# Kernel tuning notes

Measured on AMD Instinct MI355X. Metric: run time of the kernel, lower is better.

The kernel has to match this reference:

```python
import jax, jax.numpy as jnp
import numpy as np

N0, K3, K2 = 262144, 27, 8
N1, N2 = N0 // 8, N0 // 64
CIN, C0, C1, C2 = 3, 24, 48, 96
EPS = 1e-5


def _conv_bn_relu(x, neigh, W, gamma, beta):
    # Octree sparse conv: gather neighbor features and contract with kernel.
    # x: [N, Cin], neigh: [M, K] int indices into N, W: [K, Cin, Cout]
    y = jnp.einsum('mkc,kcd->md', x[neigh], W)
    # BatchNorm1d (training-mode batch statistics) + ReLU
    mu = jnp.mean(y, axis=0)
    var = jnp.var(y, axis=0)
    y = (y - mu) * jax.lax.rsqrt(var + EPS) * gamma + beta
    return jax.nn.relu(y)


def setup_inputs() -> dict:
    key = jax.random.key(0)
    k = jax.random.split(key, 16)

    def w(kk, shape, fan):
        return jax.random.normal(kk, shape, jnp.float32) / np.float32(np.sqrt(fan))

    return {
        'data':   jax.random.normal(k[0], (N0, CIN), jnp.float32),
        'neigh0': jax.random.randint(k[1], (N0, K3), 0, N0, jnp.int32),
        'child0': jax.random.randint(k[2], (N1, K2), 0, N0, jnp.int32),
        'neigh1': jax.random.randint(k[3], (N1, K3), 0, N1, jnp.int32),
        'child1': jax.random.randint(k[4], (N2, K2), 0, N1, jnp.int32),
        'neigh2': jax.random.randint(k[5], (N2, K3), 0, N2, jnp.int32),
        'w0':  w(k[6],  (K3, CIN, C0), K3 * CIN),
        'g0':  jnp.ones((C0,), jnp.float32),  'b0':  jnp.zeros((C0,), jnp.float32),
        'wd0': w(k[7],  (K2, C0, C1),  K2 * C0),
        'gd0': jnp.ones((C1,), jnp.float32),  'bd0': jnp.zeros((C1,), jnp.float32),
        'w1':  w(k[8],  (K3, C1, C1),  K3 * C1),
        'g1':  jnp.ones((C1,), jnp.float32),  'b1':  jnp.zeros((C1,), jnp.float32),
        'wd1': w(k[9],  (K2, C1, C2),  K2 * C1),
        'gd1': jnp.ones((C2,), jnp.float32),  'bd1': jnp.zeros((C2,), jnp.float32),
        'wp':  w(k[10], (K3, C2, C2),  K3 * C2),
        'gp':  jnp.ones((C2,), jnp.float32),  'bp':  jnp.zeros((C2,), jnp.float32),
    }


def reference(data, neigh0, child0, neigh1, child1, neigh2,
              w0, g0, b0, wd0, gd0, bd0, w1, g1, b1, wd1, gd1, bd1, wp, gp, bp):
    # stage 0 at depth d: conv3 then stride-2 downsample
    x = _conv_bn_relu(data, neigh0, w0, g0, b0)      # [N0, 24]
    x = _conv_bn_relu(x, child0, wd0, gd0, bd0)      # [N1, 48]
    # stage 1 at depth d-1
    x = _conv_bn_relu(x, neigh1, w1, g1, b1)         # [N1, 48]
    x = _conv_bn_relu(x, child1, wd1, gd1, bd1)      # [N2, 96]
    # proj at depth d-2
    x = _conv_bn_relu(x, neigh2, wp, gp, bp)         # [N2, 96]
    return x
```

## Files before the change

### kernel.cpp

```cpp
#include <hip/hip_runtime.h>

#define N0 262144
#define N1 32768
#define N2 4096
#define EPSBN 1e-5f

typedef unsigned short ush_t;
typedef __bf16 bf16x8 __attribute__((ext_vector_type(8)));
typedef float  f32x4  __attribute__((ext_vector_type(4)));

union ufcast { unsigned int u; float f; };
__device__ __forceinline__ float bflo(unsigned int p) { ufcast x; x.u = p << 16;          return x.f; }
__device__ __forceinline__ float bfhi(unsigned int p) { ufcast x; x.u = p & 0xffff0000u; return x.f; }
__device__ __forceinline__ ush_t f2bf(float f) {
    ufcast x; x.f = f;
    unsigned int u = x.u + 0x7fffu + ((x.u >> 16) & 1u);
    return (ush_t)(u >> 16);
}
__device__ __forceinline__ bf16x8 as_bf8(uint4 u) {
    union { uint4 u; bf16x8 b; } x; x.u = u; return x.b;
}

template<int C, int NB>
__device__ __forceinline__ void compute_ss(const float* __restrict__ bins,
                                           const float* __restrict__ g, const float* __restrict__ b,
                                           float M, float* ssl)
{
    const int tid = threadIdx.x;
    if (tid < 2 * C) {
        float s = 0.f;
#pragma unroll
        for (int k = 0; k < NB; ++k) s += bins[k * 2 * C + tid];
        ssl[tid] = s;
    }
    __syncthreads();
    if (tid < C) {
        const float mu  = ssl[tid] / M;
        const float var = fmaxf(ssl[C + tid] / M - mu * mu, 0.f);
        const float sc  = g[tid] / sqrtf(var + EPSBN);
        const float sh  = b[tid] - mu * sc;
        ssl[tid] = sc; ssl[C + tid] = sh;
    }
    __syncthreads();
}

template<int K, int CIN, int CINP_W, int COUT, int COUTP, int NCH>
__device__ __forceinline__ void prep_stage(const float* __restrict__ W, ush_t* __restrict__ Wb, int e) {
    const int k  = e & 31;
    const int n  = (e >> 5) % COUTP;
    const int ch = e / (32 * COUTP);
    const int kp = ch * 32 + k;
    const int t  = kp / CINP_W;
    const int c  = kp % CINP_W;
    float v = 0.f;
    if (t < K && c < CIN && n < COUT) v = W[((size_t)t * CIN + c) * COUT + n];
    Wb[e] = f2bf(v);
}

#define BINS_TOTAL 9984

__global__ __launch_bounds__(256) void prep_all(
    const float* w0, const float* wd0, const float* w1, const float* wd1, const float* wp,
    const float* data,
    ush_t* wbA, ush_t* wbB, ush_t* wbC, ush_t* wbD, ush_t* wbE, ush_t* xa, float* binsz)
{
    const int e = blockIdx.x * 256 + threadIdx.x;
    switch (blockIdx.y) {
        case 0: if (e <   4096) prep_stage<27,  3,  4, 24, 32,  4>(w0,  wbA, e); break;
        case 1: if (e <  12288) prep_stage< 8, 24, 32, 48, 48,  8>(wd0, wbB, e); break;
        case 2: if (e <  64512) prep_stage<27, 48, 48, 48, 48, 42>(w1,  wbC, e); break;
        case 3: if (e <  49152) prep_stage< 8, 48, 64, 96, 96, 16>(wd1, wbD, e); break;
        case 4: if (e < 248832) prep_stage<27, 96, 96, 96, 96, 81>(wp,  wbE, e); break;
        case 5: if (e < N0) {
            const float* dp = data + (size_t)3 * e;
            unsigned int h0 = f2bf(dp[0]), h1 = f2bf(dp[1]), h2 = f2bf(dp[2]);
            uint2 v; v.x = h0 | (h1 << 16); v.y = h2;
            ((uint2*)xa)[e] = v;
        } break;
        case 6: if (e < BINS_TOTAL) binsz[e] = 0.f; break;
    }
}

__global__ __launch_bounds__(256, 4) void mconvA_s(
    const ush_t* __restrict__ xa,
    const int*   __restrict__ neigh,
    const ush_t* __restrict__ Wb,
    ush_t*       __restrict__ y,
    float*       __restrict__ bins)
{
    __shared__ int   nl[3456];
    __shared__ float lsq[48];
    __shared__ ush_t ytile[128 * 24];
    const int tid = threadIdx.x;
    const int block0 = blockIdx.x * 128;

    {
        const uint4* src = (const uint4*)(neigh + (size_t)block0 * 27);
        uint4* dst = (uint4*)nl;
        for (int i = tid; i < 864; i += 256) dst[i] = src[i];
    }
    if (tid < 48) lsq[tid] = 0.f;
    __syncthreads();

    const int lane = tid & 63, wave = tid >> 6;
    const int quad = lane >> 4, l15 = lane & 15;

    uint4 au[2][4];
#pragma unroll
    for (int g = 0; g < 2; ++g) {
        const int lr = g * 64 + wave * 16 + l15;
#pragma unroll
        for (int ch = 0; ch < 4; ++ch) {
            const int tA = ch * 8 + quad * 2;
            uint4 a = make_uint4(0, 0, 0, 0);
            if (ch < 3) {
                const uint2 lo = ((const uint2*)xa)[nl[lr * 27 + tA]];
                const uint2 hi = ((const uint2*)xa)[nl[lr * 27 + tA + 1]];
                a = make_uint4(lo.x, lo.y, hi.x, hi.y);
            } else {
                if (quad == 0) {
                    const uint2 lo = ((const uint2*)xa)[nl[lr * 27 + 24]];
                    const uint2 hi = ((const uint2*)xa)[nl[lr * 27 + 25]];
                    a = make_uint4(lo.x, lo.y, hi.x, hi.y);
                } else if (quad == 1) {
                    const uint2 lo = ((const uint2*)xa)[nl[lr * 27 + 26]];
                    a = make_uint4(lo.x, lo.y, 0, 0);
                }
            }
            au[g][ch] = a;
        }
    }
    __builtin_amdgcn_sched_barrier(0);

    f32x4 acc[2][2] = {};
#pragma unroll
    for (int g = 0; g < 2; ++g)
#pragma unroll
    for (int ch = 0; ch < 4; ++ch) {
        const bf16x8 af = as_bf8(au[g][ch]);
#pragma unroll
        for (int ct = 0; ct < 2; ++ct) {
            const int n = ct * 16 + l15;
            const uint4 bu = *(const uint4*)(Wb + ((size_t)ch * 32 + n) * 32 + quad * 8);
            acc[g][ct] = __builtin_amdgcn_mfma_f32_16x16x32_bf16(af, as_bf8(bu), acc[g][ct], 0, 0, 0);
        }
    }

#pragma unroll
    for (int g = 0; g < 2; ++g)
#pragma unroll
    for (int ct = 0; ct < 2; ++ct) {
        const int col = ct * 16 + l15;
        if (col < 24) {
            float s = 0.f, q = 0.f;
#pragma unroll
            for (int r = 0; r < 4; ++r) {
                const float v = acc[g][ct][r];
                ytile[(g * 64 + wave * 16 + quad * 4 + r) * 24 + col] = f2bf(v);
                s += v; q += v * v;
            }
            atomicAdd(&lsq[col], s);
            atomicAdd(&lsq[24 + col], q);
        }
    }
    __syncthreads();

    {
        const uint4* t4 = (const uint4*)ytile;
        uint4* dst = (uint4*)(y + (size_t)block0 * 24);
        for (int i = tid; i < 384; i += 256) dst[i] = t4[i];
    }
    if (tid < 48) atomicAdd(&bins[(blockIdx.x & 15) * 48 + tid], lsq[tid]);
}

__global__ __launch_bounds__(256) void mconvB_s(
    const ush_t* __restrict__ y0,
    const float* __restrict__ bins0,
    const float* __restrict__ g, const float* __restrict__ b,
    const int*   __restrict__ child,
    const ush_t* __restrict__ Wb,
    ush_t*       __restrict__ y1b,
    float*       __restrict__ bins1)
{
    __shared__ float ssl[48];
    __shared__ float lsq[96];
    __shared__ ush_t ytile[64 * 48];
    const int tid = threadIdx.x;
    if (tid < 96) lsq[tid] = 0.f;
    compute_ss<24, 16>(bins0, g, b, (float)N0, ssl);

    const int lane = tid & 63, wave = tid >> 6;
    const int quad = lane >> 4, l15 = lane & 15;
    const int rowA = blockIdx.x * 64 + wave * 16 + l15;
    const int c0 = quad * 8;

    float sc[8], sh[8];
    if (c0 < 24) {
#pragma unroll
        for (int j = 0; j < 8; ++j) { sc[j] = ssl[c0 + j]; sh[j] = ssl[24 + c0 + j]; }
    }

    const int4 c4a = *(const int4*)(child + (size_t)rowA * 8);
    const int4 c4b = *(const int4*)(child + (size_t)rowA * 8 + 4);
    const int idxs[8] = {c4a.x, c4a.y, c4a.z, c4a.w, c4b.x, c4b.y, c4b.z, c4b.w};

    f32x4 acc[3] = {};
#pragma unroll
    for (int ci = 0; ci < 8; ++ci) {
        const int idx = idxs[ci];
        uint4 au = make_uint4(0, 0, 0, 0);
        if (c0 < 24) {
            const uint4 raw = *(const uint4*)(y0 + (size_t)idx * 24 + c0);
            const unsigned int w4[4] = {raw.x, raw.y, raw.z, raw.w};
            unsigned int o4[4];
#pragma unroll
            for (int h = 0; h < 4; ++h) {
                const float a0 = fmaxf(bflo(w4[h]) * sc[2 * h]     + sh[2 * h],     0.f);
                const float a1 = fmaxf(bfhi(w4[h]) * sc[2 * h + 1] + sh[2 * h + 1], 0.f);
                o4[h] = (unsigned)f2bf(a0) | ((unsigned)f2bf(a1) << 16);
            }
            au = make_uint4(o4[0], o4[1], o4[2], o4[3]);
        }
        const bf16x8 af = as_bf8(au);
#pragma unroll
        for (int ct = 0; ct < 3; ++ct) {
            const int n = ct * 16 + l15;
            const uint4 bu = *(const uint4*)(Wb + ((size_t)ci * 48 + n) * 32 + quad * 8);
            acc[ct] = __builtin_amdgcn_mfma_f32_16x16x32_bf16(af, as_bf8(bu), acc[ct], 0, 0, 0);
        }
    }

#pragma unroll
    for (int ct = 0; ct < 3; ++ct) {
        const int col = ct * 16 + l15;
        float s = 0.f, q = 0.f;
#pragma unroll
        for (int r = 0; r < 4; ++r) {
            const float v = acc[ct][r];
            ytile[(wave * 16 + quad * 4 + r) * 48 + col] = f2bf(v);
            s += v; q += v * v;
        }
        atomicAdd(&lsq[col], s);
        atomicAdd(&lsq[48 + col], q);
    }
    __syncthreads();

    {
        const uint4* t4 = (const uint4*)ytile;
        uint4* dst = (uint4*)(y1b + (size_t)blockIdx.x * 64 * 48);
        for (int i = tid; i < 384; i += 256) dst[i] = t4[i];
    }
    if (tid < 96) atomicAdd(&bins1[(blockIdx.x & 15) * 96 + tid], lsq[tid]);
}

__global__ __launch_bounds__(256) void mconvC_s(
    const ush_t* __restrict__ y1b,
    const float* __restrict__ bins1,
    const float* __restrict__ g, const float* __restrict__ b,
    const int*   __restrict__ neigh,
    const ush_t* __restrict__ Wb,
    float*       __restrict__ y2,
    float*       __restrict__ bins2)
{
    __shared__ float ssl[96];
    __shared__ float lsq[96];
    __shared__ int   nl[1728];
    __shared__ float tile[64 * 48];
    const int tid = threadIdx.x;
    if (tid < 96) lsq[tid] = 0.f;

    {
        const uint4* src = (const uint4*)(neigh + (size_t)blockIdx.x * 1728);
        uint4* dst = (uint4*)nl;
        for (int i = tid; i < 432; i += 256) dst[i] = src[i];
    }
    compute_ss<48, 16>(bins1, g, b, (float)N1, ssl);

    const int lane = tid & 63, wave = tid >> 6;
    const int quad = lane >> 4, l15 = lane & 15;
    const int rl = wave * 16 + l15;

    int coffs[3], tofs[3];
    float sc[3][8], sh[3][8];
#pragma unroll
    for (int m3 = 0; m3 < 3; ++m3) {
        const int gg = 32 * m3 + 8 * quad;
        coffs[m3] = gg % 48;
        tofs[m3]  = gg / 48;
#pragma unroll
        for (int j = 0; j < 8; ++j) { sc[m3][j] = ssl[coffs[m3] + j]; sh[m3][j] = ssl[48 + coffs[m3] + j]; }
    }

    f32x4 acc[3] = {};
    for (int cg = 0; cg < 14; ++cg) {
#pragma unroll
        for (int m3 = 0; m3 < 3; ++m3) {
            const int ch = 3 * cg + m3;
            int t = 2 * cg + tofs[m3];
            if (t > 26) t = 26;
            const int idx = nl[rl * 27 + t];
            const uint4 raw = *(const uint4*)(y1b + (size_t)idx * 48 + coffs[m3]);
            const unsigned int w4[4] = {raw.x, raw.y, raw.z, raw.w};
            unsigned int o4[4];
#pragma unroll
            for (int h = 0; h < 4; ++h) {
                const float a0 = fmaxf(bflo(w4[h]) * sc[m3][2 * h]     + sh[m3][2 * h],     0.f);
                const float a1 = fmaxf(bfhi(w4[h]) * sc[m3][2 * h + 1] + sh[m3][2 * h + 1], 0.f);
                o4[h] = (unsigned)f2bf(a0) | ((unsigned)f2bf(a1) << 16);
            }
            const bf16x8 af = as_bf8(make_uint4(o4[0], o4[1], o4[2], o4[3]));
#pragma unroll
            for (int ct = 0; ct < 3; ++ct) {
                const int n = ct * 16 + l15;
                const uint4 bu = *(const uint4*)(Wb + ((size_t)ch * 48 + n) * 32 + quad * 8);
                acc[ct] = __builtin_amdgcn_mfma_f32_16x16x32_bf16(af, as_bf8(bu), acc[ct], 0, 0, 0);
            }
        }
    }

#pragma unroll
    for (int ct = 0; ct < 3; ++ct) {
        const int col = ct * 16 + l15;
        float s = 0.f, q = 0.f;
#pragma unroll
        for (int r = 0; r < 4; ++r) {
            const float v = acc[ct][r];
            tile[(wave * 16 + quad * 4 + r) * 48 + col] = v;
            s += v; q += v * v;
        }
        atomicAdd(&lsq[col], s);
        atomicAdd(&lsq[48 + col], q);
    }
    __syncthreads();

    {
        const uint4* t4 = (const uint4*)tile;
        uint4* dst = (uint4*)(y2 + (size_t)blockIdx.x * 64 * 48);
        for (int i = tid; i < 768; i += 256) dst[i] = t4[i];
    }
    if (tid < 96) atomicAdd(&bins2[(blockIdx.x & 15) * 96 + tid], lsq[tid]);
}

__global__ __launch_bounds__(256) void mconvD_s(
    const float* __restrict__ y2, const float* __restrict__ bins2,
    const float* __restrict__ g, const float* __restrict__ b,
    const int*   __restrict__ child,
    const ush_t* __restrict__ Wb,
    float*       __restrict__ y3,
    float*       __restrict__ bins3)
{
    __shared__ float ssl[96];
    __shared__ float tile[16 * 96];
    const int tid = threadIdx.x;
    for (int i = tid; i < 1536; i += 256) tile[i] = 0.f;
    compute_ss<48, 16>(bins2, g, b, (float)N1, ssl);

    const int lane = tid & 63, wave = tid >> 6;
    const int quad = lane >> 4, l15 = lane & 15;
    const int rowA = blockIdx.x * 16 + l15;

    const int2 c2 = *(const int2*)(child + (size_t)rowA * 8 + wave * 2);

    f32x4 acc[6] = {};
#pragma unroll
    for (int u = 0; u < 4; ++u) {
        const int ci = wave * 4 + u;
        const int sub = ci & 1;
        const int idx = (u >> 1) ? c2.y : c2.x;
        const int c0 = sub * 32 + quad * 8;
        uint4 au = make_uint4(0, 0, 0, 0);
        if (c0 < 48) {
            const float4 v0 = *(const float4*)(y2 + (size_t)idx * 48 + c0);
            const float4 v1 = *(const float4*)(y2 + (size_t)idx * 48 + c0 + 4);
            const float vv[8] = {v0.x, v0.y, v0.z, v0.w, v1.x, v1.y, v1.z, v1.w};
            unsigned int o4[4];
#pragma unroll
            for (int h = 0; h < 4; ++h) {
                const float a0 = fmaxf(vv[2 * h]     * ssl[c0 + 2 * h]     + ssl[48 + c0 + 2 * h],     0.f);
                const float a1 = fmaxf(vv[2 * h + 1] * ssl[c0 + 2 * h + 1] + ssl[48 + c0 + 2 * h + 1], 0.f);
                o4[h] = (unsigned)f2bf(a0) | ((unsigned)f2bf(a1) << 16);
            }
            au = make_uint4(o4[0], o4[1], o4[2], o4[3]);
        }
        const bf16x8 af = as_bf8(au);
#pragma unroll
        for (int ct = 0; ct < 6; ++ct) {
            const int n = ct * 16 + l15;
            const uint4 bu = *(const uint4*)(Wb + ((size_t)ci * 96 + n) * 32 + quad * 8);
            acc[ct] = __builtin_amdgcn_mfma_f32_16x16x32_bf16(af, as_bf8(bu), acc[ct], 0, 0, 0);
        }
    }

#pragma unroll
    for (int ct = 0; ct < 6; ++ct)
#pragma unroll
        for (int r = 0; r < 4; ++r)
            atomicAdd(&tile[(quad * 4 + r) * 96 + ct * 16 + l15], acc[ct][r]);
    __syncthreads();

    const size_t row0 = (size_t)blockIdx.x * 16;
    for (int i = tid; i < 1536; i += 256) y3[row0 * 96 + i] = tile[i];
    if (tid < 96) {
        float s = 0.f, q = 0.f;
#pragma unroll
        for (int r = 0; r < 16; ++r) { const float v = tile[r * 96 + tid]; s += v; q += v * v; }
        atomicAdd(&bins3[(blockIdx.x & 15) * 192 + tid], s);
        atomicAdd(&bins3[(blockIdx.x & 15) * 192 + 96 + tid], q);
    }
}

__global__ __launch_bounds__(256) void mconvE_s(
    const float* __restrict__ y3, const float* __restrict__ bins3,
    const float* __restrict__ g, const float* __restrict__ b,
    const int*   __restrict__ neigh,
    const ush_t* __restrict__ Wb,
    float*       __restrict__ y4,
    float*       __restrict__ bins4)
{
    __shared__ float ssl[192];
    __shared__ float tile[16 * 96];
    __shared__ int   nl[432];
    const int tid = threadIdx.x;
    for (int i = tid; i < 1536; i += 256) tile[i] = 0.f;

    {
        const uint4* src = (const uint4*)(neigh + (size_t)blockIdx.x * 432);
        uint4* dst = (uint4*)nl;
        for (int i = tid; i < 108; i += 256) dst[i] = src[i];
    }
    compute_ss<96, 16>(bins3, g, b, (float)N2, ssl);

    const int lane = tid & 63, wave = tid >> 6;
    const int quad = lane >> 4, l15 = lane & 15;

    const int ci0 = (wave == 0) ? 0 : 21 + (wave - 1) * 20;
    const int cnt = (wave == 0) ? 21 : 20;

    f32x4 acc[6] = {};
    for (int u = 0; u < cnt; ++u) {
        const int ci = ci0 + u;
        const int t = ci / 3, sub = ci % 3;
        const int idx = nl[l15 * 27 + t];
        const int c0 = sub * 32 + quad * 8;
        const float4 v0 = *(const float4*)(y3 + (size_t)idx * 96 + c0);
        const float4 v1 = *(const float4*)(y3 + (size_t)idx * 96 + c0 + 4);
        const float vv[8] = {v0.x, v0.y, v0.z, v0.w, v1.x, v1.y, v1.z, v1.w};
        unsigned int o4[4];
#pragma unroll
        for (int h = 0; h < 4; ++h) {
            const float a0 = fmaxf(vv[2 * h]     * ssl[c0 + 2 * h]     + ssl[96 + c0 + 2 * h],     0.f);
            const float a1 = fmaxf(vv[2 * h + 1] * ssl[c0 + 2 * h + 1] + ssl[96 + c0 + 2 * h + 1], 0.f);
            o4[h] = (unsigned)f2bf(a0) | ((unsigned)f2bf(a1) << 16);
        }
        const bf16x8 af = as_bf8(make_uint4(o4[0], o4[1], o4[2], o4[3]));
#pragma unroll
        for (int ct = 0; ct < 6; ++ct) {
            const int n = ct * 16 + l15;
            const uint4 bu = *(const uint4*)(Wb + ((size_t)ci * 96 + n) * 32 + quad * 8);
            acc[ct] = __builtin_amdgcn_mfma_f32_16x16x32_bf16(af, as_bf8(bu), acc[ct], 0, 0, 0);
        }
    }

#pragma unroll
    for (int ct = 0; ct < 6; ++ct)
#pragma unroll
        for (int r = 0; r < 4; ++r)
            atomicAdd(&tile[(quad * 4 + r) * 96 + ct * 16 + l15], acc[ct][r]);
    __syncthreads();

    const size_t row0 = (size_t)blockIdx.x * 16;
    for (int i = tid; i < 1536; i += 256) y4[row0 * 96 + i] = tile[i];
    if (tid < 96) {
        float s = 0.f, q = 0.f;
#pragma unroll
        for (int r = 0; r < 16; ++r) { const float v = tile[r * 96 + tid]; s += v; q += v * v; }
        atomicAdd(&bins4[(blockIdx.x & 15) * 192 + tid], s);
        atomicAdd(&bins4[(blockIdx.x & 15) * 192 + 96 + tid], q);
    }
}

__global__ __launch_bounds__(256) void writeout_s(
    const float* __restrict__ y4, const float* __restrict__ bins4,
    const float* __restrict__ g, const float* __restrict__ b,
    float* __restrict__ out)
{
    __shared__ float ssl[192];
    compute_ss<96, 16>(bins4, g, b, (float)N2, ssl);

    const int i = (blockIdx.x * 256 + threadIdx.x) * 4;
    const int c = i % 96;
    float4 v = *(const float4*)(y4 + i);
    float4 o;
    o.x = fmaxf(v.x * ssl[c + 0] + ssl[96 + c + 0], 0.f);
    o.y = fmaxf(v.y * ssl[c + 1] + ssl[96 + c + 1], 0.f);
    o.z = fmaxf(v.z * ssl[c + 2] + ssl[96 + c + 2], 0.f);
    o.w = fmaxf(v.w * ssl[c + 3] + ssl[96 + c + 3], 0.f);
    *(float4*)(out + i) = o;
}

extern "C" void kernel_launch(void* const* d_in, const int* in_sizes, int n_in,
                              void* d_out, int out_size, void* d_ws, size_t ws_size,
                              hipStream_t stream)
{
    const float* data   = (const float*)d_in[0];
    const int*   neigh0 = (const int*)d_in[1];
    const int*   child0 = (const int*)d_in[2];
    const int*   neigh1 = (const int*)d_in[3];
    const int*   child1 = (const int*)d_in[4];
    const int*   neigh2 = (const int*)d_in[5];
    const float* w0  = (const float*)d_in[6];
    const float* g0  = (const float*)d_in[7];
    const float* b0  = (const float*)d_in[8];
    const float* wd0 = (const float*)d_in[9];
    const float* gd0 = (const float*)d_in[10];
    const float* bd0 = (const float*)d_in[11];
    const float* w1  = (const float*)d_in[12];
    const float* g1  = (const float*)d_in[13];
    const float* b1  = (const float*)d_in[14];
    const float* wd1 = (const float*)d_in[15];
    const float* gd1 = (const float*)d_in[16];
    const float* bd1 = (const float*)d_in[17];
    const float* wp  = (const float*)d_in[18];
    const float* gp  = (const float*)d_in[19];
    const float* bp  = (const float*)d_in[20];
    float* out = (float*)d_out;

    float* wsf = (float*)d_ws;
    float* bins0 = wsf;
    float* bins1 = wsf + 768;
    float* bins2 = wsf + 2304;
    float* bins3 = wsf + 3840;
    float* bins4 = wsf + 6912;

    float* Y2  = wsf + 10240;
    float* Y3  = Y2 + (size_t)1572864;
    float* Y4  = Y3 + (size_t)393216;
    ush_t* Y0B = (ush_t*)(Y4 + (size_t)393216);
    ush_t* Y1B = Y0B + (size_t)6291456;
    ush_t* XA  = Y1B + (size_t)1572864;
    ush_t* WB  = XA + (size_t)1048576;

    ush_t* wbA = WB;
    ush_t* wbB = WB + 4096;
    ush_t* wbC = WB + 16384;
    ush_t* wbD = WB + 80896;
    ush_t* wbE = WB + 130048;

    prep_all<<<dim3(1024, 7), 256, 0, stream>>>(w0, wd0, w1, wd1, wp, data,
                                                wbA, wbB, wbC, wbD, wbE, XA, wsf);

    mconvA_s<<<N0 / 128, 256, 0, stream>>>(XA, neigh0, wbA, Y0B, bins0);
    mconvB_s<<<N1 / 64, 256, 0, stream>>>(Y0B, bins0, g0, b0, child0, wbB, Y1B, bins1);
    mconvC_s<<<N1 / 64, 256, 0, stream>>>(Y1B, bins1, gd0, bd0, neigh1, wbC, Y2, bins2);
    mconvD_s<<<N2 / 16, 256, 0, stream>>>(Y2, bins2, g1, b1, child1, wbD, Y3, bins3);
    mconvE_s<<<N2 / 16, 256, 0, stream>>>(Y3, bins3, gd1, bd1, neigh2, wbE, Y4, bins4);
    writeout_s<<<N2 * 96 / 4 / 256, 256, 0, stream>>>(Y4, bins4, gp, bp, out);

    (void)in_sizes; (void)n_in; (void)out_size; (void)ws_size;
}
```

Measured before the change: 237.0 us.

## Merge later conv stages into cooperative kernels with grid-wide syncs

Replaces five separate launches (mconvB..E and writeout) with two cooperative kernels that use grid.sync() between stages, so batch-norm statistics are visible without a kernel boundary. The aim is to remove launch and drain gaps between the small late stages. It also removes a sched_barrier in mconvA. Cooperative launch requires the whole grid to be co-resident (512 blocks of 256 threads here). If the grid cannot be resident the launch fails, and grid syncs carry their own cost.

```diff
diff --git a/kernel.cpp b/kernel.cpp
--- a/kernel.cpp
+++ b/kernel.cpp
@@ -1,4 +1,7 @@
 #include <hip/hip_runtime.h>
+#include <hip/hip_cooperative_groups.h>
+
+namespace cg = cooperative_groups;
 
 #define N0 262144
 #define N1 32768
@@ -130,7 +133,6 @@
             au[g][ch] = a;
         }
     }
-    __builtin_amdgcn_sched_barrier(0);
 
     f32x4 acc[2][2] = {};
 #pragma unroll
@@ -173,329 +175,327 @@
     if (tid < 48) atomicAdd(&bins[(blockIdx.x & 15) * 48 + tid], lsq[tid]);
 }
 
-__global__ __launch_bounds__(256) void mconvB_s(
+__global__ __launch_bounds__(256) void coopBC(
     const ush_t* __restrict__ y0,
     const float* __restrict__ bins0,
-    const float* __restrict__ g, const float* __restrict__ b,
+    const float* __restrict__ gB, const float* __restrict__ bB,
     const int*   __restrict__ child,
-    const ush_t* __restrict__ Wb,
+    const ush_t* __restrict__ WbB,
     ush_t*       __restrict__ y1b,
-    float*       __restrict__ bins1)
-{
-    __shared__ float ssl[48];
-    __shared__ float lsq[96];
-    __shared__ ush_t ytile[64 * 48];
-    const int tid = threadIdx.x;
-    if (tid < 96) lsq[tid] = 0.f;
-    compute_ss<24, 16>(bins0, g, b, (float)N0, ssl);
-
-    const int lane = tid & 63, wave = tid >> 6;
-    const int quad = lane >> 4, l15 = lane & 15;
-    const int rowA = blockIdx.x * 64 + wave * 16 + l15;
-    const int c0 = quad * 8;
-
-    float sc[8], sh[8];
-    if (c0 < 24) {
-#pragma unroll
-        for (int j = 0; j < 8; ++j) { sc[j] = ssl[c0 + j]; sh[j] = ssl[24 + c0 + j]; }
-    }
-
-    const int4 c4a = *(const int4*)(child + (size_t)rowA * 8);
-    const int4 c4b = *(const int4*)(child + (size_t)rowA * 8 + 4);
-    const int idxs[8] = {c4a.x, c4a.y, c4a.z, c4a.w, c4b.x, c4b.y, c4b.z, c4b.w};
-
-    f32x4 acc[3] = {};
-#pragma unroll
-    for (int ci = 0; ci < 8; ++ci) {
-        const int idx = idxs[ci];
-        uint4 au = make_uint4(0, 0, 0, 0);
-        if (c0 < 24) {
-            const uint4 raw = *(const uint4*)(y0 + (size_t)idx * 24 + c0);
-            const unsigned int w4[4] = {raw.x, raw.y, raw.z, raw.w};
-            unsigned int o4[4];
-#pragma unroll
-            for (int h = 0; h < 4; ++h) {
-                const float a0 = fmaxf(bflo(w4[h]) * sc[2 * h]     + sh[2 * h],     0.f);
-                const float a1 = fmaxf(bfhi(w4[h]) * sc[2 * h + 1] + sh[2 * h + 1], 0.f);
-                o4[h] = (unsigned)f2bf(a0) | ((unsigned)f2bf(a1) << 16);
-            }
-            au = make_uint4(o4[0], o4[1], o4[2], o4[3]);
-        }
-        const bf16x8 af = as_bf8(au);
-#pragma unroll
-        for (int ct = 0; ct < 3; ++ct) {
-            const int n = ct * 16 + l15;
-            const uint4 bu = *(const uint4*)(Wb + ((size_t)ci * 48 + n) * 32 + quad * 8);
-            acc[ct] = __builtin_amdgcn_mfma_f32_16x16x32_bf16(af, as_bf8(bu), acc[ct], 0, 0, 0);
-        }
-    }
-
-#pragma unroll
-    for (int ct = 0; ct < 3; ++ct) {
-        const int col = ct * 16 + l15;
-        float s = 0.f, q = 0.f;
-#pragma unroll
-        for (int r = 0; r < 4; ++r) {
-            const float v = acc[ct][r];
-            ytile[(wave * 16 + quad * 4 + r) * 48 + col] = f2bf(v);
-            s += v; q += v * v;
-        }
-        atomicAdd(&lsq[col], s);
-        atomicAdd(&lsq[48 + col], q);
-    }
-    __syncthreads();
-
-    {
-        const uint4* t4 = (const uint4*)ytile;
-        uint4* dst = (uint4*)(y1b + (size_t)blockIdx.x * 64 * 48);
-        for (int i = tid; i < 384; i += 256) dst[i] = t4[i];
-    }
-    if (tid < 96) atomicAdd(&bins1[(blockIdx.x & 15) * 96 + tid], lsq[tid]);
-}
-
-__global__ __launch_bounds__(256) void mconvC_s(
-    const ush_t* __restrict__ y1b,
-    const float* __restrict__ bins1,
-    const float* __restrict__ g, const float* __restrict__ b,
+    float*       __restrict__ bins1,
+    const float* __restrict__ gC, const float* __restrict__ bC,
     const int*   __restrict__ neigh,
-    const ush_t* __restrict__ Wb,
+    const ush_t* __restrict__ WbC,
     float*       __restrict__ y2,
     float*       __restrict__ bins2)
 {
-    __shared__ float ssl[96];
-    __shared__ float lsq[96];
+    __shared__ float sslB[48];
+    __shared__ float lsqB[96];
+    __shared__ ush_t ytile[64 * 48];
+    __shared__ float sslC[96];
+    __shared__ float lsqC[96];
     __shared__ int   nl[1728];
     __shared__ float tile[64 * 48];
+
     const int tid = threadIdx.x;
-    if (tid < 96) lsq[tid] = 0.f;
-
-    {
-        const uint4* src = (const uint4*)(neigh + (size_t)blockIdx.x * 1728);
-        uint4* dst = (uint4*)nl;
-        for (int i = tid; i < 432; i += 256) dst[i] = src[i];
-    }
-    compute_ss<48, 16>(bins1, g, b, (float)N1, ssl);
-
     const int lane = tid & 63, wave = tid >> 6;
     const int quad = lane >> 4, l15 = lane & 15;
-    const int rl = wave * 16 + l15;
-
-    int coffs[3], tofs[3];
-    float sc[3][8], sh[3][8];
-#pragma unroll
-    for (int m3 = 0; m3 < 3; ++m3) {
-        const int gg = 32 * m3 + 8 * quad;
-        coffs[m3] = gg % 48;
-        tofs[m3]  = gg / 48;
-#pragma unroll
-        for (int j = 0; j < 8; ++j) { sc[m3][j] = ssl[coffs[m3] + j]; sh[m3][j] = ssl[48 + coffs[m3] + j]; }
-    }
-
-    f32x4 acc[3] = {};
-    for (int cg = 0; cg < 14; ++cg) {
-#pragma unroll
-        for (int m3 = 0; m3 < 3; ++m3) {
-            const int ch = 3 * cg + m3;
-            int t = 2 * cg + tofs[m3];
-            if (t > 26) t = 26;
-            const int idx = nl[rl * 27 + t];
-            const uint4 raw = *(const uint4*)(y1b + (size_t)idx * 48 + coffs[m3]);
-            const unsigned int w4[4] = {raw.x, raw.y, raw.z, raw.w};
-            unsigned int o4[4];
-#pragma unroll
-            for (int h = 0; h < 4; ++h) {
-                const float a0 = fmaxf(bflo(w4[h]) * sc[m3][2 * h]     + sh[m3][2 * h],     0.f);
-                const float a1 = fmaxf(bfhi(w4[h]) * sc[m3][2 * h + 1] + sh[m3][2 * h + 1], 0.f);
-                o4[h] = (unsigned)f2bf(a0) | ((unsigned)f2bf(a1) << 16);
-            }
-            const bf16x8 af = as_bf8(make_uint4(o4[0], o4[1], o4[2], o4[3]));
+
+    {
+        if (tid < 96) lsqB[tid] = 0.f;
+        compute_ss<24, 16>(bins0, gB, bB, (float)N0, sslB);
+
+        const int rowA = blockIdx.x * 64 + wave * 16 + l15;
+        const int c0 = quad * 8;
+
+        float sc[8], sh[8];
+        if (c0 < 24) {
+#pragma unroll
+            for (int j = 0; j < 8; ++j) { sc[j] = sslB[c0 + j]; sh[j] = sslB[24 + c0 + j]; }
+        }
+
+        const int4 c4a = *(const int4*)(child + (size_t)rowA * 8);
+        const int4 c4b = *(const int4*)(child + (size_t)rowA * 8 + 4);
+        const int idxs[8] = {c4a.x, c4a.y, c4a.z, c4a.w, c4b.x, c4b.y, c4b.z, c4b.w};
+
+        f32x4 acc[3] = {};
+#pragma unroll
+        for (int ci = 0; ci < 8; ++ci) {
+            const int idx = idxs[ci];
+            uint4 au = make_uint4(0, 0, 0, 0);
+            if (c0 < 24) {
+                const uint4 raw = *(const uint4*)(y0 + (size_t)idx * 24 + c0);
+                const unsigned int w4[4] = {raw.x, raw.y, raw.z, raw.w};
+                unsigned int o4[4];
+#pragma unroll
+                for (int h = 0; h < 4; ++h) {
+                    const float a0 = fmaxf(bflo(w4[h]) * sc[2 * h]     + sh[2 * h],     0.f);
+                    const float a1 = fmaxf(bfhi(w4[h]) * sc[2 * h + 1] + sh[2 * h + 1], 0.f);
+                    o4[h] = (unsigned)f2bf(a0) | ((unsigned)f2bf(a1) << 16);
+                }
+                au = make_uint4(o4[0], o4[1], o4[2], o4[3]);
+            }
+            const bf16x8 af = as_bf8(au);
 #pragma unroll
             for (int ct = 0; ct < 3; ++ct) {
                 const int n = ct * 16 + l15;
-                const uint4 bu = *(const uint4*)(Wb + ((size_t)ch * 48 + n) * 32 + quad * 8);
+                const uint4 bu = *(const uint4*)(WbB + ((size_t)ci * 48 + n) * 32 + quad * 8);
                 acc[ct] = __builtin_amdgcn_mfma_f32_16x16x32_bf16(af, as_bf8(bu), acc[ct], 0, 0, 0);
             }
         }
-    }
-
-#pragma unroll
-    for (int ct = 0; ct < 3; ++ct) {
-        const int col = ct * 16 + l15;
-        float s = 0.f, q = 0.f;
-#pragma unroll
-        for (int r = 0; r < 4; ++r) {
-            const float v = acc[ct][r];
-            tile[(wave * 16 + quad * 4 + r) * 48 + col] = v;
-            s += v; q += v * v;
-        }
-        atomicAdd(&lsq[col], s);
-        atomicAdd(&lsq[48 + col], q);
-    }
-    __syncthreads();
-
-    {
-        const uint4* t4 = (const uint4*)tile;
-        uint4* dst = (uint4*)(y2 + (size_t)blockIdx.x * 64 * 48);
-        for (int i = tid; i < 768; i += 256) dst[i] = t4[i];
-    }
-    if (tid < 96) atomicAdd(&bins2[(blockIdx.x & 15) * 96 + tid], lsq[tid]);
-}
-
-__global__ __launch_bounds__(256) void mconvD_s(
+
+#pragma unroll
+        for (int ct = 0; ct < 3; ++ct) {
+            const int col = ct * 16 + l15;
+            float s = 0.f, q = 0.f;
+#pragma unroll
+            for (int r = 0; r < 4; ++r) {
+                const float v = acc[ct][r];
+                ytile[(wave * 16 + quad * 4 + r) * 48 + col] = f2bf(v);
+                s += v; q += v * v;
+            }
+            atomicAdd(&lsqB[col], s);
+            atomicAdd(&lsqB[48 + col], q);
+        }
+        __syncthreads();
+
+        {
+            const uint4* t4 = (const uint4*)ytile;
+            uint4* dst = (uint4*)(y1b + (size_t)blockIdx.x * 64 * 48);
+            for (int i = tid; i < 384; i += 256) dst[i] = t4[i];
+        }
+        if (tid < 96) atomicAdd(&bins1[(blockIdx.x & 15) * 96 + tid], lsqB[tid]);
+    }
+
+    cg::this_grid().sync();
+
+    {
+        if (tid < 96) lsqC[tid] = 0.f;
+
+        {
+            const uint4* src = (const uint4*)(neigh + (size_t)blockIdx.x * 1728);
+            uint4* dst = (uint4*)nl;
+            for (int i = tid; i < 432; i += 256) dst[i] = src[i];
+        }
+        compute_ss<48, 16>(bins1, gC, bC, (float)N1, sslC);
+
+        const int rl = wave * 16 + l15;
+
+        int coffs[3], tofs[3];
+        float sc[3][8], sh[3][8];
+#pragma unroll
+        for (int m3 = 0; m3 < 3; ++m3) {
+            const int gg = 32 * m3 + 8 * quad;
+            coffs[m3] = gg % 48;
+            tofs[m3]  = gg / 48;
+#pragma unroll
+            for (int j = 0; j < 8; ++j) { sc[m3][j] = sslC[coffs[m3] + j]; sh[m3][j] = sslC[48 + coffs[m3] + j]; }
+        }
+
+        f32x4 acc[3] = {};
+        for (int cg2 = 0; cg2 < 14; ++cg2) {
+#pragma unroll
+            for (int m3 = 0; m3 < 3; ++m3) {
+                const int ch = 3 * cg2 + m3;
+                int t = 2 * cg2 + tofs[m3];
+                if (t > 26) t = 26;
+                const int idx = nl[rl * 27 + t];
+                const uint4 raw = *(const uint4*)(y1b + (size_t)idx * 48 + coffs[m3]);
+                const unsigned int w4[4] = {raw.x, raw.y, raw.z, raw.w};
+                unsigned int o4[4];
+#pragma unroll
+                for (int h = 0; h < 4; ++h) {
+                    const float a0 = fmaxf(bflo(w4[h]) * sc[m3][2 * h]     + sh[m3][2 * h],     0.f);
+                    const float a1 = fmaxf(bfhi(w4[h]) * sc[m3][2 * h + 1] + sh[m3][2 * h + 1], 0.f);
+                    o4[h] = (unsigned)f2bf(a0) | ((unsigned)f2bf(a1) << 16);
+                }
+                const bf16x8 af = as_bf8(make_uint4(o4[0], o4[1], o4[2], o4[3]));
+#pragma unroll
+                for (int ct = 0; ct < 3; ++ct) {
+                    const int n = ct * 16 + l15;
+                    const uint4 bu = *(const uint4*)(WbC + ((size_t)ch * 48 + n) * 32 + quad * 8);
+                    acc[ct] = __builtin_amdgcn_mfma_f32_16x16x32_bf16(af, as_bf8(bu), acc[ct], 0, 0, 0);
+                }
+            }
+        }
+
+#pragma unroll
+        for (int ct = 0; ct < 3; ++ct) {
+            const int col = ct * 16 + l15;
+            float s = 0.f, q = 0.f;
+#pragma unroll
+            for (int r = 0; r < 4; ++r) {
+                const float v = acc[ct][r];
+                tile[(wave * 16 + quad * 4 + r) * 48 + col] = v;
+                s += v; q += v * v;
+            }
+            atomicAdd(&lsqC[col], s);
+            atomicAdd(&lsqC[48 + col], q);
+        }
+        __syncthreads();
+
+        {
+            const uint4* t4 = (const uint4*)tile;
+            uint4* dst = (uint4*)(y2 + (size_t)blockIdx.x * 64 * 48);
+            for (int i = tid; i < 768; i += 256) dst[i] = t4[i];
+        }
+        if (tid < 96) atomicAdd(&bins2[(blockIdx.x & 15) * 96 + tid], lsqC[tid]);
+    }
+}
+
+__global__ __launch_bounds__(256) void coopDEW(
     const float* __restrict__ y2, const float* __restrict__ bins2,
-    const float* __restrict__ g, const float* __restrict__ b,
+    const float* __restrict__ gD, const float* __restrict__ bD,
     const int*   __restrict__ child,
-    const ush_t* __restrict__ Wb,
+    const ush_t* __restrict__ WbD,
     float*       __restrict__ y3,
-    float*       __restrict__ bins3)
-{
-    __shared__ float ssl[96];
-    __shared__ float tile[16 * 96];
-    const int tid = threadIdx.x;
-    for (int i = tid; i < 1536; i += 256) tile[i] = 0.f;
-    compute_ss<48, 16>(bins2, g, b, (float)N1, ssl);
-
-    const int lane = tid & 63, wave = tid >> 6;
-    const int quad = lane >> 4, l15 = lane & 15;
-    const int rowA = blockIdx.x * 16 + l15;
-
-    const int2 c2 = *(const int2*)(child + (size_t)rowA * 8 + wave * 2);
-
-    f32x4 acc[6] = {};
-#pragma unroll
-    for (int u = 0; u < 4; ++u) {
-        const int ci = wave * 4 + u;
-        const int sub = ci & 1;
-        const int idx = (u >> 1) ? c2.y : c2.x;
-        const int c0 = sub * 32 + quad * 8;
-        uint4 au = make_uint4(0, 0, 0, 0);
-        if (c0 < 48) {
-            const float4 v0 = *(const float4*)(y2 + (size_t)idx * 48 + c0);
-            const float4 v1 = *(const float4*)(y2 + (size_t)idx * 48 + c0 + 4);
-            const float vv[8] = {v0.x, v0.y, v0.z, v0.w, v1.x, v1.y, v1.z, v1.w};
-            unsigned int o4[4];
-#pragma unroll
-            for (int h = 0; h < 4; ++h) {
-                const float a0 = fmaxf(vv[2 * h]     * ssl[c0 + 2 * h]     + ssl[48 + c0 + 2 * h],     0.f);
-                const float a1 = fmaxf(vv[2 * h + 1] * ssl[c0 + 2 * h + 1] + ssl[48 + c0 + 2 * h + 1], 0.f);
-                o4[h] = (unsigned)f2bf(a0) | ((unsigned)f2bf(a1) << 16);
-            }
-            au = make_uint4(o4[0], o4[1], o4[2], o4[3]);
-        }
-        const bf16x8 af = as_bf8(au);
-#pragma unroll
-        for (int ct = 0; ct < 6; ++ct) {
-            const int n = ct * 16 + l15;
-            const uint4 bu = *(const uint4*)(Wb + ((size_t)ci * 96 + n) * 32 + quad * 8);
-            acc[ct] = __builtin_amdgcn_mfma_f32_16x16x32_bf16(af, as_bf8(bu), acc[ct], 0, 0, 0);
-        }
-    }
-
-#pragma unroll
-    for (int ct = 0; ct < 6; ++ct)
-#pragma unroll
-        for (int r = 0; r < 4; ++r)
-            atomicAdd(&tile[(quad * 4 + r) * 96 + ct * 16 + l15], acc[ct][r]);
-    __syncthreads();
-
-    const size_t row0 = (size_t)blockIdx.x * 16;
-    for (int i = tid; i < 1536; i += 256) y3[row0 * 96 + i] = tile[i];
-    if (tid < 96) {
-        float s = 0.f, q = 0.f;
-#pragma unroll
-        for (int r = 0; r < 16; ++r) { const float v = tile[r * 96 + tid]; s += v; q += v * v; }
-        atomicAdd(&bins3[(blockIdx.x & 15) * 192 + tid], s);
-        atomicAdd(&bins3[(blockIdx.x & 15) * 192 + 96 + tid], q);
-    }
-}
-
-__global__ __launch_bounds__(256) void mconvE_s(
-    const float* __restrict__ y3, const float* __restrict__ bins3,
-    const float* __restrict__ g, const float* __restrict__ b,
+    float*       __restrict__ bins3,
+    const float* __restrict__ gE, const float* __restrict__ bE,
     const int*   __restrict__ neigh,
-    const ush_t* __restrict__ Wb,
+    const ush_t* __restrict__ WbE,
     float*       __restrict__ y4,
-    float*       __restrict__ bins4)
+    float*       __restrict__ bins4,
+    const float* __restrict__ gW, const float* __restrict__ bW,
+    float*       __restrict__ out)
 {
     __shared__ float ssl[192];
     __shared__ float tile[16 * 96];
     __shared__ int   nl[432];
+
     const int tid = threadIdx.x;
-    for (int i = tid; i < 1536; i += 256) tile[i] = 0.f;
-
-    {
-        const uint4* src = (const uint4*)(neigh + (size_t)blockIdx.x * 432);
-        uint4* dst = (uint4*)nl;
-        for (int i = tid; i < 108; i += 256) dst[i] = src[i];
-    }
-    compute_ss<96, 16>(bins3, g, b, (float)N2, ssl);
-
     const int lane = tid & 63, wave = tid >> 6;
     const int quad = lane >> 4, l15 = lane & 15;
 
-    const int ci0 = (wave == 0) ? 0 : 21 + (wave - 1) * 20;
-    const int cnt = (wave == 0) ? 21 : 20;
-
-    f32x4 acc[6] = {};
-    for (int u = 0; u < cnt; ++u) {
-        const int ci = ci0 + u;
-        const int t = ci / 3, sub = ci % 3;
-        const int idx = nl[l15 * 27 + t];
-        const int c0 = sub * 32 + quad * 8;
-        const float4 v0 = *(const float4*)(y3 + (size_t)idx * 96 + c0);
-        const float4 v1 = *(const float4*)(y3 + (size_t)idx * 96 + c0 + 4);
-        const float vv[8] = {v0.x, v0.y, v0.z, v0.w, v1.x, v1.y, v1.z, v1.w};
-        unsigned int o4[4];
-#pragma unroll
-        for (int h = 0; h < 4; ++h) {
-            const float a0 = fmaxf(vv[2 * h]     * ssl[c0 + 2 * h]     + ssl[96 + c0 + 2 * h],     0.f);
-            const float a1 = fmaxf(vv[2 * h + 1] * ssl[c0 + 2 * h + 1] + ssl[96 + c0 + 2 * h + 1], 0.f);
-            o4[h] = (unsigned)f2bf(a0) | ((unsigned)f2bf(a1) << 16);
-        }
-        const bf16x8 af = as_bf8(make_uint4(o4[0], o4[1], o4[2], o4[3]));
-#pragma unroll
-        for (int ct = 0; ct < 6; ++ct) {
-            const int n = ct * 16 + l15;
-            const uint4 bu = *(const uint4*)(Wb + ((size_t)ci * 96 + n) * 32 + quad * 8);
-            acc[ct] = __builtin_amdgcn_mfma_f32_16x16x32_bf16(af, as_bf8(bu), acc[ct], 0, 0, 0);
-        }
-    }
-
-#pragma unroll
-    for (int ct = 0; ct < 6; ++ct)
-#pragma unroll
-        for (int r = 0; r < 4; ++r)
-            atomicAdd(&tile[(quad * 4 + r) * 96 + ct * 16 + l15], acc[ct][r]);
-    __syncthreads();
-
-    const size_t row0 = (size_t)blockIdx.x * 16;
-    for (int i = tid; i < 1536; i += 256) y4[row0 * 96 + i] = tile[i];
-    if (tid < 96) {
-        float s = 0.f, q = 0.f;
-#pragma unroll
-        for (int r = 0; r < 16; ++r) { const float v = tile[r * 96 + tid]; s += v; q += v * v; }
-        atomicAdd(&bins4[(blockIdx.x & 15) * 192 + tid], s);
-        atomicAdd(&bins4[(blockIdx.x & 15) * 192 + 96 + tid], q);
-    }
-}
-
-__global__ __launch_bounds__(256) void writeout_s(
-    const float* __restrict__ y4, const float* __restrict__ bins4,
-    const float* __restrict__ g, const float* __restrict__ b,
-    float* __restrict__ out)
-{
-    __shared__ float ssl[192];
-    compute_ss<96, 16>(bins4, g, b, (float)N2, ssl);
-
-    const int i = (blockIdx.x * 256 + threadIdx.x) * 4;
-    const int c = i % 96;
-    float4 v = *(const float4*)(y4 + i);
-    float4 o;
-    o.x = fmaxf(v.x * ssl[c + 0] + ssl[96 + c + 0], 0.f);
-    o.y = fmaxf(v.y * ssl[c + 1] + ssl[96 + c + 1], 0.f);
-    o.z = fmaxf(v.z * ssl[c + 2] + ssl[96 + c + 2], 0.f);
-    o.w = fmaxf(v.w * ssl[c + 3] + ssl[96 + c + 3], 0.f);
-    *(float4*)(out + i) = o;
+    {
+        for (int i = tid; i < 1536; i += 256) tile[i] = 0.f;
+        compute_ss<48, 16>(bins2, gD, bD, (float)N1, ssl);
+
+        const int rowA = blockIdx.x * 16 + l15;
+        const int2 c2 = *(const int2*)(child + (size_t)rowA * 8 + wave * 2);
+
+        f32x4 acc[6] = {};
+#pragma unroll
+        for (int u = 0; u < 4; ++u) {
+            const int ci = wave * 4 + u;
+            const int sub = ci & 1;
+            const int idx = (u >> 1) ? c2.y : c2.x;
+            const int c0 = sub * 32 + quad * 8;
+            uint4 au = make_uint4(0, 0, 0, 0);
+            if (c0 < 48) {
+                const float4 v0 = *(const float4*)(y2 + (size_t)idx * 48 + c0);
+                const float4 v1 = *(const float4*)(y2 + (size_t)idx * 48 + c0 + 4);
+                const float vv[8] = {v0.x, v0.y, v0.z, v0.w, v1.x, v1.y, v1.z, v1.w};
+                unsigned int o4[4];
+#pragma unroll
+                for (int h = 0; h < 4; ++h) {
+                    const float a0 = fmaxf(vv[2 * h]     * ssl[c0 + 2 * h]     + ssl[48 + c0 + 2 * h],     0.f);
+                    const float a1 = fmaxf(vv[2 * h + 1] * ssl[c0 + 2 * h + 1] + ssl[48 + c0 + 2 * h + 1], 0.f);
+                    o4[h] = (unsigned)f2bf(a0) | ((unsigned)f2bf(a1) << 16);
+                }
+                au = make_uint4(o4[0], o4[1], o4[2], o4[3]);
+            }
+            const bf16x8 af = as_bf8(au);
+#pragma unroll
+            for (int ct = 0; ct < 6; ++ct) {
+                const int n = ct * 16 + l15;
+                const uint4 bu = *(const uint4*)(WbD + ((size_t)ci * 96 + n) * 32 + quad * 8);
+                acc[ct] = __builtin_amdgcn_mfma_f32_16x16x32_bf16(af, as_bf8(bu), acc[ct], 0, 0, 0);
+            }
+        }
+
+#pragma unroll
+        for (int ct = 0; ct < 6; ++ct)
+#pragma unroll
+            for (int r = 0; r < 4; ++r)
+                atomicAdd(&tile[(quad * 4 + r) * 96 + ct * 16 + l15], acc[ct][r]);
+        __syncthreads();
+
+        const size_t row0 = (size_t)blockIdx.x * 16;
+        for (int i = tid; i < 1536; i += 256) y3[row0 * 96 + i] = tile[i];
+        if (tid < 96) {
+            float s = 0.f, q = 0.f;
+#pragma unroll
+            for (int r = 0; r < 16; ++r) { const float v = tile[r * 96 + tid]; s += v; q += v * v; }
+            atomicAdd(&bins3[(blockIdx.x & 15) * 192 + tid], s);
+            atomicAdd(&bins3[(blockIdx.x & 15) * 192 + 96 + tid], q);
+        }
+    }
+
+    cg::this_grid().sync();
+
+    {
+        for (int i = tid; i < 1536; i += 256) tile[i] = 0.f;
+
+        {
+            const uint4* src = (const uint4*)(neigh + (size_t)blockIdx.x * 432);
+            uint4* dst = (uint4*)nl;
+            for (int i = tid; i < 108; i += 256) dst[i] = src[i];
+        }
+        compute_ss<96, 16>(bins3, gE, bE, (float)N2, ssl);
+
+        const int ci0 = (wave == 0) ? 0 : 21 + (wave - 1) * 20;
+        const int cnt = (wave == 0) ? 21 : 20;
+
+        f32x4 acc[6] = {};
+        for (int u = 0; u < cnt; ++u) {
+            const int ci = ci0 + u;
+            const int t = ci / 3, sub = ci % 3;
+            const int idx = nl[l15 * 27 + t];
+            const int c0 = sub * 32 + quad * 8;
+            const float4 v0 = *(const float4*)(y3 + (size_t)idx * 96 + c0);
+            const float4 v1 = *(const float4*)(y3 + (size_t)idx * 96 + c0 + 4);
+            const float vv[8] = {v0.x, v0.y, v0.z, v0.w, v1.x, v1.y, v1.z, v1.w};
+            unsigned int o4[4];
+#pragma unroll
+            for (int h = 0; h < 4; ++h) {
+                const float a0 = fmaxf(vv[2 * h]     * ssl[c0 + 2 * h]     + ssl[96 + c0 + 2 * h],     0.f);
+                const float a1 = fmaxf(vv[2 * h + 1] * ssl[c0 + 2 * h + 1] + ssl[96 + c0 + 2 * h + 1], 0.f);
+                o4[h] = (unsigned)f2bf(a0) | ((unsigned)f2bf(a1) << 16);
+            }
+            const bf16x8 af = as_bf8(make_uint4(o4[0], o4[1], o4[2], o4[3]));
+#pragma unroll
+            for (int ct = 0; ct < 6; ++ct) {
+                const int n = ct * 16 + l15;
+                const uint4 bu = *(const uint4*)(WbE + ((size_t)ci * 96 + n) * 32 + quad * 8);
+                acc[ct] = __builtin_amdgcn_mfma_f32_16x16x32_bf16(af, as_bf8(bu), acc[ct], 0, 0, 0);
+            }
+        }
+
+#pragma unroll
+        for (int ct = 0; ct < 6; ++ct)
+#pragma unroll
+            for (int r = 0; r < 4; ++r)
+                atomicAdd(&tile[(quad * 4 + r) * 96 + ct * 16 + l15], acc[ct][r]);
+        __syncthreads();
+
+        const size_t row0 = (size_t)blockIdx.x * 16;
+        for (int i = tid; i < 1536; i += 256) y4[row0 * 96 + i] = tile[i];
+        if (tid < 96) {
+            float s = 0.f, q = 0.f;
+#pragma unroll
+            for (int r = 0; r < 16; ++r) { const float v = tile[r * 96 + tid]; s += v; q += v * v; }
+            atomicAdd(&bins4[(blockIdx.x & 15) * 192 + tid], s);
+            atomicAdd(&bins4[(blockIdx.x & 15) * 192 + 96 + tid], q);
+        }
+    }
+
+    cg::this_grid().sync();
+
+    {
+        compute_ss<96, 16>(bins4, gW, bW, (float)N2, ssl);
+
+        for (int i = tid; i < 384; i += 256) {
+            const int gi = blockIdx.x * 384 + i;
+            const int c = (gi % 24) * 4;
+            const float4 v = ((const float4*)y4)[gi];
+            float4 o;
+            o.x = fmaxf(v.x * ssl[c + 0] + ssl[96 + c + 0], 0.f);
+            o.y = fmaxf(v.y * ssl[c + 1] + ssl[96 + c + 1], 0.f);
+            o.z = fmaxf(v.z * ssl[c + 2] + ssl[96 + c + 2], 0.f);
+            o.w = fmaxf(v.w * ssl[c + 3] + ssl[96 + c + 3], 0.f);
+            ((float4*)out)[gi] = o;
+        }
+    }
 }
 
 extern "C" void kernel_launch(void* const* d_in, const int* in_sizes, int n_in,
@@ -550,11 +550,29 @@
                                                 wbA, wbB, wbC, wbD, wbE, XA, wsf);
 
     mconvA_s<<<N0 / 128, 256, 0, stream>>>(XA, neigh0, wbA, Y0B, bins0);
-    mconvB_s<<<N1 / 64, 256, 0, stream>>>(Y0B, bins0, g0, b0, child0, wbB, Y1B, bins1);
-    mconvC_s<<<N1 / 64, 256, 0, stream>>>(Y1B, bins1, gd0, bd0, neigh1, wbC, Y2, bins2);
-    mconvD_s<<<N2 / 16, 256, 0, stream>>>(Y2, bins2, g1, b1, child1, wbD, Y3, bins3);
-    mconvE_s<<<N2 / 16, 256, 0, stream>>>(Y3, bins3, gd1, bd1, neigh2, wbE, Y4, bins4);
-    writeout_s<<<N2 * 96 / 4 / 256, 256, 0, stream>>>(Y4, bins4, gp, bp, out);
+
+    {
+        void* args[] = {
+            (void*)&Y0B, (void*)&bins0, (void*)&g0, (void*)&b0,
+            (void*)&child0, (void*)&wbB, (void*)&Y1B, (void*)&bins1,
+            (void*)&gd0, (void*)&bd0, (void*)&neigh1, (void*)&wbC,
+            (void*)&Y2, (void*)&bins2
+        };
+        hipLaunchCooperativeKernel((const void*)coopBC, dim3(N1 / 64), dim3(256),
+                                   args, 0, stream);
+    }
+
+    {
+        void* args[] = {
+            (void*)&Y2, (void*)&bins2, (void*)&g1, (void*)&b1,
+            (void*)&child1, (void*)&wbD, (void*)&Y3, (void*)&bins3,
+            (void*)&gd1, (void*)&bd1, (void*)&neigh2, (void*)&wbE,
+            (void*)&Y4, (void*)&bins4,
+            (void*)&gp, (void*)&bp, (void*)&out
+        };
+        hipLaunchCooperativeKernel((const void*)coopDEW, dim3(N2 / 16), dim3(256),
+                                   args, 0, stream);
+    }
 
     (void)in_sizes; (void)n_in; (void)out_size; (void)ws_size;
 }
```

Result: slower. 365.2 us (+54.1%).
